# Kernel optimization log

Measured on AMD Instinct MI355X. Metric: run time of the kernel, lower is better.

The kernel has to match this reference:

```python
import jax, jax.numpy as jnp
import numpy as np

B, N = 8, 50000
DIM, C_DIM, TASK_DIM, H, NB, OUT = 3, 64, 512, 64, 5, 12


def setup_inputs() -> dict:
    key = jax.random.key(0)
    ks = jax.random.split(key, 16)
    s = lambda fan_in: 1.0 / np.sqrt(fan_in)
    inp = {
        "p": jax.random.normal(ks[0], (B, N, DIM), dtype=jnp.float32),
        "c": jax.random.normal(ks[1], (B, N, C_DIM), dtype=jnp.float32),
        "task_feature": jax.random.normal(ks[2], (B, TASK_DIM), dtype=jnp.float32),
        # params (stored as [in, out] so y = x @ W + b)
        "fc_p_W": jax.random.uniform(ks[3], (DIM, H), jnp.float32, -s(DIM), s(DIM)),
        "fc_p_b": jax.random.uniform(ks[4], (H,), jnp.float32, -s(DIM), s(DIM)),
        "fc_c_W": jax.random.uniform(ks[5], (NB, C_DIM + TASK_DIM, H), jnp.float32, -s(C_DIM + TASK_DIM), s(C_DIM + TASK_DIM)),
        "fc_c_b": jax.random.uniform(ks[6], (NB, H), jnp.float32, -s(C_DIM + TASK_DIM), s(C_DIM + TASK_DIM)),
        "blk0_W": jax.random.uniform(ks[7], (NB, H, H), jnp.float32, -s(H), s(H)),
        "blk0_b": jax.random.uniform(ks[8], (NB, H), jnp.float32, -s(H), s(H)),
        "blk1_W": jax.random.uniform(ks[9], (NB, H, H), jnp.float32, -s(H), s(H)) * 0.1,
        "blk1_b": jax.random.uniform(ks[10], (NB, H), jnp.float32, -s(H), s(H)),
        "fc_out_W": jax.random.uniform(ks[11], (H, OUT), jnp.float32, -s(H), s(H)),
        "fc_out_b": jax.random.uniform(ks[12], (OUT,), jnp.float32, -s(H), s(H)),
    }
    return inp


def reference(p, c, task_feature, fc_p_W, fc_p_b, fc_c_W, fc_c_b,
              blk0_W, blk0_b, blk1_W, blk1_b, fc_out_W, fc_out_b):
    b, n = p.shape[0], p.shape[1]
    # expand task feature to every point and concat with point-wise code c
    tf = jnp.broadcast_to(task_feature[:, None, :], (b, n, task_feature.shape[-1]))
    cc = jnp.concatenate([c, tf], axis=-1)              # [B, N, 576]
    net = p @ fc_p_W + fc_p_b                           # [B, N, H]
    for i in range(fc_c_W.shape[0]):
        net = net + cc @ fc_c_W[i] + fc_c_b[i]          # conditioning
        # ResnetBlockFC: dx = fc_1(relu(fc_0(relu(x)))); out = x + dx
        h = jax.nn.relu(net) @ blk0_W[i] + blk0_b[i]
        dx = jax.nn.relu(h) @ blk1_W[i] + blk1_b[i]
        net = net + dx
    out = jax.nn.relu(net) @ fc_out_W + fc_out_b        # [B, N, 12]
    return out
```

## Files before the change

kernel.cpp:

```cpp
#include <hip/hip_runtime.h>

#define B_    8
#define N_    50000
#define NB_   5
#define OUT_  12
#define THREADS 256
#define TILES_ 4
#define PTS_PER_BLOCK (TILES_ * 16 * 4)
#define BLOCKS_PER_BATCH ((N_ + PTS_PER_BLOCK - 1) / PTS_PER_BLOCK)

typedef _Float16 half8 __attribute__((ext_vector_type(8)));
typedef float   floatx4 __attribute__((ext_vector_type(4)));

__device__ __forceinline__ half8 ldg8(const _Float16* p) {
    union { uint4 u; half8 h; } x;
    x.u = *(const uint4*)p;
    return x.h;
}

__device__ __forceinline__ half8 packB(floatx4 a, floatx4 b) {
    half8 r;
    r[0] = (_Float16)fmaxf(a[0], 0.f); r[1] = (_Float16)fmaxf(a[1], 0.f);
    r[2] = (_Float16)fmaxf(a[2], 0.f); r[3] = (_Float16)fmaxf(a[3], 0.f);
    r[4] = (_Float16)fmaxf(b[0], 0.f); r[5] = (_Float16)fmaxf(b[1], 0.f);
    r[6] = (_Float16)fmaxf(b[2], 0.f); r[7] = (_Float16)fmaxf(b[3], 0.f);
    return r;
}

__global__ void task_proj_kernel(const float* __restrict__ tf,
                                 const float* __restrict__ fc_c_W,
                                 const float* __restrict__ fc_c_b,
                                 const float* __restrict__ fc_p_b,
                                 float* __restrict__ tp_out) {
    __shared__ float partial[4][64];
    int bi = blockIdx.x;
    int b = bi / NB_, i = bi % NB_;
    int j = threadIdx.x & 63;
    int g = threadIdx.x >> 6;
    const float* W  = fc_c_W + ((size_t)i * 576 + 64) * 64;
    const float* tb = tf + b * 512;
    float acc = 0.f;
    int t0 = g * 128;
    #pragma unroll 8
    for (int t = 0; t < 128; ++t)
        acc += tb[t0 + t] * W[(size_t)(t0 + t) * 64 + j];
    partial[g][j] = acc;
    __syncthreads();
    if (g == 0) {
        float s = partial[0][j] + partial[1][j] + partial[2][j] + partial[3][j]
                + fc_c_b[i * 64 + j];
        if (i == 0) s += fc_p_b[j];
        tp_out[(b * NB_ + i) * 64 + j] = s;
    }
}

__global__ void prep_weights(const float* __restrict__ fc_c_W,
                             const float* __restrict__ blk0_W,
                             const float* __restrict__ blk1_W,
                             const float* __restrict__ fc_out_W,
                             _Float16* __restrict__ ws_w,
                             _Float16* __restrict__ ws_fco) {
    int u = blockIdx.x * THREADS + threadIdx.x;
    if (u < 7680) {
        int m15 = u & 15, q = (u >> 4) & 3, h = (u >> 6) & 1, T = (u >> 7) & 3;
        int mi = u >> 9;
        int mat = mi / 5, i = mi % 5;
        int n = T * 16 + m15;
        _Float16 out[8];
        #pragma unroll
        for (int j = 0; j < 8; ++j) {
            float v;
            if (mat == 0) {
                int k = 32 * h + 8 * q + j;
                v = fc_c_W[((size_t)i * 576 + k) * 64 + n];
            } else {
                int f = 32 * h + 16 * (j >> 2) + 4 * q + (j & 3);
                const float* W = (mat == 1) ? blk0_W : blk1_W;
                v = W[((size_t)i * 64 + f) * 64 + n];
            }
            out[j] = (_Float16)v;
        }
        *(uint4*)(ws_w + (size_t)u * 8) = *(uint4*)out;
    } else if (u < 7808) {
        int e = u - 7680;
        int m15 = e & 15, q = (e >> 4) & 3, h = (e >> 6) & 1;
        _Float16 out[8];
        #pragma unroll
        for (int j = 0; j < 8; ++j) {
            int f = 32 * h + 16 * (j >> 2) + 4 * q + (j & 3);
            out[j] = (m15 < OUT_) ? (_Float16)fc_out_W[f * OUT_ + m15] : (_Float16)0.f;
        }
        *(uint4*)(ws_fco + (size_t)e * 8) = *(uint4*)out;
    }
}

__global__ __launch_bounds__(THREADS, 2) void decoder_kernel(
    const float* __restrict__ p_g, const float* __restrict__ c_g,
    const float* __restrict__ blk0_b, const float* __restrict__ blk1_b,
    const float* __restrict__ fc_p_W, const float* __restrict__ fc_out_b,
    const _Float16* __restrict__ ws_w, const _Float16* __restrict__ ws_fco,
    const float* __restrict__ ws_tp, float* __restrict__ out_g)
{
    __shared__ float fpw_l[192];
    __shared__ float b0_l[NB_ * 64];
    __shared__ float b1_l[NB_ * 64];
    __shared__ float tp_l[NB_ * 64];
    __shared__ float fob_l[16];

    const int tid   = threadIdx.x;
    const int batch = blockIdx.x / BLOCKS_PER_BATCH;
    const int blk   = blockIdx.x % BLOCKS_PER_BATCH;
    const int base  = blk * PTS_PER_BLOCK;
    const int npts  = min(PTS_PER_BLOCK, N_ - base);
    const int ntiles = npts >> 4;
    const long gbase = (long)batch * N_ + base;

    if (tid < 192) fpw_l[tid] = fc_p_W[tid];
    for (int u = tid; u < NB_ * 64; u += THREADS) {
        b0_l[u] = blk0_b[u];
        b1_l[u] = blk1_b[u];
        tp_l[u] = ws_tp[batch * (NB_ * 64) + u];
    }
    if (tid < 16) fob_l[tid] = (tid < OUT_) ? fc_out_b[tid] : 0.f;
    __syncthreads();

    const int lane = tid & 63;
    const int wv   = tid >> 6;
    const int q    = lane >> 4;
    const int m15  = lane & 15;

    int tileid[TILES_];
    bool act[TILES_];
    #pragma unroll
    for (int t = 0; t < TILES_; ++t) {
        tileid[t] = wv + 4 * t;
        act[t] = (tileid[t] < ntiles);
    }

    half8 cB[TILES_][2];
    #pragma unroll
    for (int t = 0; t < TILES_; ++t) {
        if (!act[t]) continue;
        const float* cr = c_g + (size_t)(gbase + tileid[t] * 16 + m15) * 64;
        #pragma unroll
        for (int h = 0; h < 2; ++h) {
            float4 v0 = *(const float4*)(cr + 32 * h + 8 * q);
            float4 v1 = *(const float4*)(cr + 32 * h + 8 * q + 4);
            half8 r;
            r[0] = (_Float16)v0.x; r[1] = (_Float16)v0.y;
            r[2] = (_Float16)v0.z; r[3] = (_Float16)v0.w;
            r[4] = (_Float16)v1.x; r[5] = (_Float16)v1.y;
            r[6] = (_Float16)v1.z; r[7] = (_Float16)v1.w;
            cB[t][h] = r;
        }
    }

    floatx4 net4[TILES_][4];
    #pragma unroll
    for (int t = 0; t < TILES_; ++t) {
        if (!act[t]) continue;
        long g = gbase + tileid[t] * 16 + m15;
        float pp0 = p_g[g * 3 + 0], pp1 = p_g[g * 3 + 1], pp2 = p_g[g * 3 + 2];
        #pragma unroll
        for (int T = 0; T < 4; ++T) {
            #pragma unroll
            for (int r = 0; r < 4; ++r) {
                int f = (T << 4) + (q << 2) + r;
                net4[t][T][r] = pp0 * fpw_l[f] + pp1 * fpw_l[64 + f] + pp2 * fpw_l[128 + f];
            }
        }
    }

    #pragma unroll 1
    for (int i = 0; i < NB_; ++i) {
        floatx4 tpv[4], bb0[4], bb1[4];
        #pragma unroll
        for (int T = 0; T < 4; ++T) {
            int off = i * 64 + (T << 4) + (q << 2);
            tpv[T] = *(const floatx4*)(tp_l + off);
            bb0[T] = *(const floatx4*)(b0_l + off);
            bb1[T] = *(const floatx4*)(b1_l + off);
        }
        {
            const _Float16* wbase = ws_w + ((size_t)(0 * 5 + i) * 512) * 8;
            half8 A[4][2];
            #pragma unroll
            for (int T = 0; T < 4; ++T)
                #pragma unroll
                for (int h = 0; h < 2; ++h)
                    A[T][h] = ldg8(wbase + ((T * 128 + h * 64 + q * 16 + m15) * 8));
            #pragma unroll
            for (int t = 0; t < TILES_; ++t) {
                if (!act[t]) continue;
                #pragma unroll
                for (int T = 0; T < 4; ++T) {
                    floatx4 a = net4[t][T];
                    a = __builtin_amdgcn_mfma_f32_16x16x32_f16(A[T][0], cB[t][0], a, 0, 0, 0);
                    a = __builtin_amdgcn_mfma_f32_16x16x32_f16(A[T][1], cB[t][1], a, 0, 0, 0);
                    net4[t][T] = a + tpv[T];
                }
            }
        }
        {
            const _Float16* w0 = ws_w + ((size_t)(1 * 5 + i) * 512) * 8;
            const _Float16* w1 = ws_w + ((size_t)(2 * 5 + i) * 512) * 8;
            half8 A0[4][2], A1[4][2];
            #pragma unroll
            for (int T = 0; T < 4; ++T)
                #pragma unroll
                for (int h = 0; h < 2; ++h) {
                    int off = (T * 128 + h * 64 + q * 16 + m15) * 8;
                    A0[T][h] = ldg8(w0 + off);
                    A1[T][h] = ldg8(w1 + off);
                }
            #pragma unroll
            for (int t = 0; t < TILES_; ++t) {
                if (!act[t]) continue;
                half8 Bn0 = packB(net4[t][0], net4[t][1]);
                half8 Bn1 = packB(net4[t][2], net4[t][3]);
                floatx4 hh[4];
                #pragma unroll
                for (int T = 0; T < 4; ++T) {
                    floatx4 a = bb0[T];
                    a = __builtin_amdgcn_mfma_f32_16x16x32_f16(A0[T][0], Bn0, a, 0, 0, 0);
                    a = __builtin_amdgcn_mfma_f32_16x16x32_f16(A0[T][1], Bn1, a, 0, 0, 0);
                    hh[T] = a;
                }
                half8 Bh0 = packB(hh[0], hh[1]);
                half8 Bh1 = packB(hh[2], hh[3]);
                #pragma unroll
                for (int T = 0; T < 4; ++T) {
                    floatx4 a = bb1[T];
                    a = __builtin_amdgcn_mfma_f32_16x16x32_f16(A1[T][0], Bh0, a, 0, 0, 0);
                    a = __builtin_amdgcn_mfma_f32_16x16x32_f16(A1[T][1], Bh1, a, 0, 0, 0);
                    net4[t][T] += a;
                }
            }
        }
    }

    half8 Ao0 = ldg8(ws_fco + (0 * 64 + q * 16 + m15) * 8);
    half8 Ao1 = ldg8(ws_fco + (1 * 64 + q * 16 + m15) * 8);
    floatx4 ob;
    #pragma unroll
    for (int r = 0; r < 4; ++r) ob[r] = fob_l[(q << 2) + r];
    #pragma unroll
    for (int t = 0; t < TILES_; ++t) {
        if (!act[t]) continue;
        half8 Bn0 = packB(net4[t][0], net4[t][1]);
        half8 Bn1 = packB(net4[t][2], net4[t][3]);
        floatx4 a = ob;
        a = __builtin_amdgcn_mfma_f32_16x16x32_f16(Ao0, Bn0, a, 0, 0, 0);
        a = __builtin_amdgcn_mfma_f32_16x16x32_f16(Ao1, Bn1, a, 0, 0, 0);
        if (q < 3) {
            long g = gbase + tileid[t] * 16 + m15;
            *(float4*)(out_g + g * OUT_ + (q << 2)) = make_float4(a[0], a[1], a[2], a[3]);
        }
    }
}

extern "C" void kernel_launch(void* const* d_in, const int* in_sizes, int n_in,
                              void* d_out, int out_size, void* d_ws, size_t ws_size,
                              hipStream_t stream) {
    const float* p        = (const float*)d_in[0];
    const float* c        = (const float*)d_in[1];
    const float* tf       = (const float*)d_in[2];
    const float* fc_p_W   = (const float*)d_in[3];
    const float* fc_p_b   = (const float*)d_in[4];
    const float* fc_c_W   = (const float*)d_in[5];
    const float* fc_c_b   = (const float*)d_in[6];
    const float* blk0_W   = (const float*)d_in[7];
    const float* blk0_b   = (const float*)d_in[8];
    const float* blk1_W   = (const float*)d_in[9];
    const float* blk1_b   = (const float*)d_in[10];
    const float* fc_out_W = (const float*)d_in[11];
    const float* fc_out_b = (const float*)d_in[12];
    float* out = (float*)d_out;

    _Float16* ws_w   = (_Float16*)d_ws;
    _Float16* ws_fco = ws_w + 7680 * 8;
    float*    ws_tp  = (float*)(ws_fco + 128 * 8);

    prep_weights<<<31, THREADS, 0, stream>>>(fc_c_W, blk0_W, blk1_W, fc_out_W, ws_w, ws_fco);
    task_proj_kernel<<<B_ * NB_, THREADS, 0, stream>>>(tf, fc_c_W, fc_c_b, fc_p_b, ws_tp);
    decoder_kernel<<<B_ * BLOCKS_PER_BATCH, THREADS, 0, stream>>>(
        p, c, blk0_b, blk1_b, fc_p_W, fc_out_b, ws_w, ws_fco, ws_tp, out);
}
```

Measured before the change: 247.7 us.

## Restructure decoder into single-wave blocks with double-buffered weight registers and replicated weights

The decoder now runs one 64-thread wave per block with four tiles each. Weight fragments are double-buffered in registers (X/Y) so the next matrix's loads are issued while the current MFMAs run. Biases and task projections are read straight from global memory instead of staged through LDS, which removes the barrier. The fp16 weight buffer is replicated up to 8 times across workspace to spread cache traffic. The task projection is split into more blocks plus a finalize kernel merged with weight prep. This raises register pressure and adds a launch and extra workspace writes.

Result: faster. 237.3 us (-4.2%).

```diff
diff --git a/kernel.cpp b/kernel.cpp
--- a/kernel.cpp
+++ b/kernel.cpp
@@ -4,10 +4,9 @@
 #define N_    50000
 #define NB_   5
 #define OUT_  12
-#define THREADS 256
 #define TILES_ 4
-#define PTS_PER_BLOCK (TILES_ * 16 * 4)
-#define BLOCKS_PER_BATCH ((N_ + PTS_PER_BLOCK - 1) / PTS_PER_BLOCK)
+#define TILES_PER_BATCH 3125
+#define BLOCKS_PER_BATCH 782
 
 typedef _Float16 half8 __attribute__((ext_vector_type(8)));
 typedef float   floatx4 __attribute__((ext_vector_type(4)));
@@ -27,121 +26,176 @@
     return r;
 }
 
-__global__ void task_proj_kernel(const float* __restrict__ tf,
-                                 const float* __restrict__ fc_c_W,
-                                 const float* __restrict__ fc_c_b,
-                                 const float* __restrict__ fc_p_b,
-                                 float* __restrict__ tp_out) {
-    __shared__ float partial[4][64];
-    int bi = blockIdx.x;
-    int b = bi / NB_, i = bi % NB_;
-    int j = threadIdx.x & 63;
-    int g = threadIdx.x >> 6;
-    const float* W  = fc_c_W + ((size_t)i * 576 + 64) * 64;
-    const float* tb = tf + b * 512;
-    float acc = 0.f;
-    int t0 = g * 128;
-    #pragma unroll 8
-    for (int t = 0; t < 128; ++t)
-        acc += tb[t0 + t] * W[(size_t)(t0 + t) * 64 + j];
-    partial[g][j] = acc;
-    __syncthreads();
-    if (g == 0) {
-        float s = partial[0][j] + partial[1][j] + partial[2][j] + partial[3][j]
-                + fc_c_b[i * 64 + j];
-        if (i == 0) s += fc_p_b[j];
-        tp_out[(b * NB_ + i) * 64 + j] = s;
-    }
-}
-
-__global__ void prep_weights(const float* __restrict__ fc_c_W,
-                             const float* __restrict__ blk0_W,
-                             const float* __restrict__ blk1_W,
-                             const float* __restrict__ fc_out_W,
-                             _Float16* __restrict__ ws_w,
-                             _Float16* __restrict__ ws_fco) {
-    int u = blockIdx.x * THREADS + threadIdx.x;
-    if (u < 7680) {
-        int m15 = u & 15, q = (u >> 4) & 3, h = (u >> 6) & 1, T = (u >> 7) & 3;
-        int mi = u >> 9;
-        int mat = mi / 5, i = mi % 5;
-        int n = T * 16 + m15;
-        _Float16 out[8];
-        #pragma unroll
-        for (int j = 0; j < 8; ++j) {
-            float v;
-            if (mat == 0) {
-                int k = 32 * h + 8 * q + j;
-                v = fc_c_W[((size_t)i * 576 + k) * 64 + n];
-            } else {
-                int f = 32 * h + 16 * (j >> 2) + 4 * q + (j & 3);
-                const float* W = (mat == 1) ? blk0_W : blk1_W;
-                v = W[((size_t)i * 64 + f) * 64 + n];
+__device__ __forceinline__ void load8(half8 (&A)[8], const _Float16* base, int q16m) {
+    #pragma unroll
+    for (int T = 0; T < 4; ++T)
+        #pragma unroll
+        for (int h = 0; h < 2; ++h)
+            A[T * 2 + h] = ldg8(base + (size_t)(T * 128 + h * 64 + q16m) * 8);
+}
+
+__global__ void prep_kernel(const float* __restrict__ fc_c_W,
+                            const float* __restrict__ blk0_W,
+                            const float* __restrict__ blk1_W,
+                            const float* __restrict__ fc_out_W,
+                            const float* __restrict__ tf,
+                            _Float16* __restrict__ ws_w,
+                            _Float16* __restrict__ ws_fco,
+                            float* __restrict__ partials, int R) {
+    int bid = blockIdx.x, tid = threadIdx.x;
+    if (bid < 32) {
+        int u = bid * 256 + tid;
+        if (u < 7680) {
+            int m15 = u & 15, q = (u >> 4) & 3, h = (u >> 6) & 1, T = (u >> 7) & 3;
+            int mi = u >> 9;
+            int mat = mi / 5, i = mi % 5;
+            int n = T * 16 + m15;
+            _Float16 out[8];
+            #pragma unroll
+            for (int j = 0; j < 8; ++j) {
+                float v;
+                if (mat == 0) {
+                    int k = 32 * h + 8 * q + j;
+                    v = fc_c_W[((size_t)i * 576 + k) * 64 + n];
+                } else {
+                    int f = 32 * h + 16 * (j >> 2) + 4 * q + (j & 3);
+                    const float* W = (mat == 1) ? blk0_W : blk1_W;
+                    v = W[((size_t)i * 64 + f) * 64 + n];
+                }
+                out[j] = (_Float16)v;
             }
-            out[j] = (_Float16)v;
-        }
-        *(uint4*)(ws_w + (size_t)u * 8) = *(uint4*)out;
-    } else if (u < 7808) {
-        int e = u - 7680;
-        int m15 = e & 15, q = (e >> 4) & 3, h = (e >> 6) & 1;
-        _Float16 out[8];
-        #pragma unroll
-        for (int j = 0; j < 8; ++j) {
-            int f = 32 * h + 16 * (j >> 2) + 4 * q + (j & 3);
-            out[j] = (m15 < OUT_) ? (_Float16)fc_out_W[f * OUT_ + m15] : (_Float16)0.f;
-        }
-        *(uint4*)(ws_fco + (size_t)e * 8) = *(uint4*)out;
-    }
-}
-
-__global__ __launch_bounds__(THREADS, 2) void decoder_kernel(
+            uint4 val = *(uint4*)out;
+            for (int r = 0; r < R; ++r)
+                *(uint4*)(ws_w + (size_t)r * 61440 + (size_t)u * 8) = val;
+        } else {
+            int e = u - 7680;
+            _Float16 out[8] = {};
+            if (e < 128) {
+                int m15 = e & 15, q = (e >> 4) & 3, h = (e >> 6) & 1;
+                #pragma unroll
+                for (int j = 0; j < 8; ++j) {
+                    int f = 32 * h + 16 * (j >> 2) + 4 * q + (j & 3);
+                    out[j] = (m15 < OUT_) ? (_Float16)fc_out_W[f * OUT_ + m15] : (_Float16)0.f;
+                }
+            }
+            uint4 val = *(uint4*)out;
+            for (int r = 0; r < R; ++r)
+                *(uint4*)(ws_fco + (size_t)r * 4096 + (size_t)e * 8) = val;
+        }
+    } else {
+        int idx2 = bid - 32;
+        int b = idx2 / 10, rem = idx2 % 10, i = rem >> 1, hf = rem & 1;
+        int g = tid >> 6, j = tid & 63;
+        const float* W  = fc_c_W + ((size_t)i * 576 + 64) * 64;
+        const float* tb = tf + b * 512;
+        int t0 = hf * 256 + g * 64;
+        float acc = 0.f;
+        #pragma unroll 8
+        for (int t = 0; t < 64; ++t)
+            acc += tb[t0 + t] * W[(size_t)(t0 + t) * 64 + j];
+        partials[(((b * 5 + i) << 3) + (hf * 4 + g)) * 64 + j] = acc;
+    }
+}
+
+__global__ void finalize_tp(const float* __restrict__ partials,
+                            const float* __restrict__ fc_c_b,
+                            const float* __restrict__ fc_p_b,
+                            float* __restrict__ tp) {
+    int u = blockIdx.x * 256 + threadIdx.x;
+    if (u >= 2560) return;
+    int b = u / 320, rem = u % 320, i = rem >> 6, j = rem & 63;
+    float s = fc_c_b[i * 64 + j] + ((i == 0) ? fc_p_b[j] : 0.f);
+    #pragma unroll
+    for (int k = 0; k < 8; ++k)
+        s += partials[(((b * 5 + i) << 3) + k) * 64 + j];
+    tp[u] = s;
+}
+
+__device__ __forceinline__ void resblock(
+    half8 (&Ac)[8], half8 (&Ab)[8],
+    floatx4 (&net4)[TILES_][4], const half8 (&cB)[TILES_][2],
+    int tc, int i, int q, int q16m,
+    const float* __restrict__ tp_b, const float* __restrict__ b0g,
+    const float* __restrict__ b1g, const _Float16* __restrict__ wsr,
+    const _Float16* __restrict__ next_cond_base, bool last)
+{
+    floatx4 tpv[4], bb0[4], bb1[4];
+    #pragma unroll
+    for (int T = 0; T < 4; ++T) {
+        int off = i * 64 + 16 * T + 4 * q;
+        tpv[T] = *(const floatx4*)(tp_b + off);
+        bb0[T] = *(const floatx4*)(b0g + off);
+        bb1[T] = *(const floatx4*)(b1g + off);
+    }
+    #pragma unroll
+    for (int t = 0; t < TILES_; ++t) {
+        if (t >= tc) break;
+        #pragma unroll
+        for (int T = 0; T < 4; ++T) {
+            floatx4 a = net4[t][T];
+            a = __builtin_amdgcn_mfma_f32_16x16x32_f16(Ac[2 * T], cB[t][0], a, 0, 0, 0);
+            a = __builtin_amdgcn_mfma_f32_16x16x32_f16(Ac[2 * T + 1], cB[t][1], a, 0, 0, 0);
+            net4[t][T] = a + tpv[T];
+        }
+    }
+    load8(Ac, wsr + (size_t)(10 + i) * 4096, q16m);
+    #pragma unroll
+    for (int t = 0; t < TILES_; ++t) {
+        if (t >= tc) break;
+        half8 Bn0 = packB(net4[t][0], net4[t][1]);
+        half8 Bn1 = packB(net4[t][2], net4[t][3]);
+        floatx4 hh[4];
+        #pragma unroll
+        for (int T = 0; T < 4; ++T) {
+            floatx4 a = bb0[T];
+            a = __builtin_amdgcn_mfma_f32_16x16x32_f16(Ab[2 * T], Bn0, a, 0, 0, 0);
+            a = __builtin_amdgcn_mfma_f32_16x16x32_f16(Ab[2 * T + 1], Bn1, a, 0, 0, 0);
+            hh[T] = a;
+        }
+        half8 Bh0 = packB(hh[0], hh[1]);
+        half8 Bh1 = packB(hh[2], hh[3]);
+        #pragma unroll
+        for (int T = 0; T < 4; ++T) {
+            floatx4 a = bb1[T];
+            a = __builtin_amdgcn_mfma_f32_16x16x32_f16(Ac[2 * T], Bh0, a, 0, 0, 0);
+            a = __builtin_amdgcn_mfma_f32_16x16x32_f16(Ac[2 * T + 1], Bh1, a, 0, 0, 0);
+            net4[t][T] += a;
+        }
+    }
+    load8(Ab, next_cond_base, q16m);
+    if (!last)
+        load8(Ac, wsr + (size_t)(5 + i + 1) * 4096, q16m);
+}
+
+__global__ __launch_bounds__(64, 2) void decoder_kernel(
     const float* __restrict__ p_g, const float* __restrict__ c_g,
     const float* __restrict__ blk0_b, const float* __restrict__ blk1_b,
     const float* __restrict__ fc_p_W, const float* __restrict__ fc_out_b,
     const _Float16* __restrict__ ws_w, const _Float16* __restrict__ ws_fco,
-    const float* __restrict__ ws_tp, float* __restrict__ out_g)
+    const float* __restrict__ tp_g, float* __restrict__ out_g, int rmask)
 {
-    __shared__ float fpw_l[192];
-    __shared__ float b0_l[NB_ * 64];
-    __shared__ float b1_l[NB_ * 64];
-    __shared__ float tp_l[NB_ * 64];
-    __shared__ float fob_l[16];
-
-    const int tid   = threadIdx.x;
-    const int batch = blockIdx.x / BLOCKS_PER_BATCH;
-    const int blk   = blockIdx.x % BLOCKS_PER_BATCH;
-    const int base  = blk * PTS_PER_BLOCK;
-    const int npts  = min(PTS_PER_BLOCK, N_ - base);
-    const int ntiles = npts >> 4;
-    const long gbase = (long)batch * N_ + base;
-
-    if (tid < 192) fpw_l[tid] = fc_p_W[tid];
-    for (int u = tid; u < NB_ * 64; u += THREADS) {
-        b0_l[u] = blk0_b[u];
-        b1_l[u] = blk1_b[u];
-        tp_l[u] = ws_tp[batch * (NB_ * 64) + u];
-    }
-    if (tid < 16) fob_l[tid] = (tid < OUT_) ? fc_out_b[tid] : 0.f;
-    __syncthreads();
-
-    const int lane = tid & 63;
-    const int wv   = tid >> 6;
-    const int q    = lane >> 4;
-    const int m15  = lane & 15;
-
-    int tileid[TILES_];
-    bool act[TILES_];
-    #pragma unroll
-    for (int t = 0; t < TILES_; ++t) {
-        tileid[t] = wv + 4 * t;
-        act[t] = (tileid[t] < ntiles);
-    }
+    const int bid   = blockIdx.x;
+    const int batch = bid / BLOCKS_PER_BATCH;
+    const int blk   = bid % BLOCKS_PER_BATCH;
+    const int tile0 = blk * TILES_;
+    const int tc    = min(TILES_, TILES_PER_BATCH - tile0);
+    const long gbase = (long)batch * N_ + (long)tile0 * 16;
+    const int lane = threadIdx.x;
+    const int q = lane >> 4, m15 = lane & 15;
+    const int q16m = q * 16 + m15;
+    const _Float16* wsr  = ws_w  + (size_t)(bid & rmask) * 61440;
+    const _Float16* fcor = ws_fco + (size_t)(bid & rmask) * 4096;
+    const float* tp_b = tp_g + batch * (NB_ * 64);
+
+    half8 X[8], Y[8];
+    load8(X, wsr, q16m);
+    load8(Y, wsr + (size_t)5 * 4096, q16m);
 
     half8 cB[TILES_][2];
     #pragma unroll
     for (int t = 0; t < TILES_; ++t) {
-        if (!act[t]) continue;
-        const float* cr = c_g + (size_t)(gbase + tileid[t] * 16 + m15) * 64;
+        if (t >= tc) break;
+        const float* cr = c_g + (size_t)(gbase + t * 16 + m15) * 64;
         #pragma unroll
         for (int h = 0; h < 2; ++h) {
             float4 v0 = *(const float4*)(cr + 32 * h + 8 * q);
@@ -155,106 +209,42 @@
         }
     }
 
+    floatx4 fw[3][4];
+    #pragma unroll
+    for (int d = 0; d < 3; ++d)
+        #pragma unroll
+        for (int T = 0; T < 4; ++T)
+            fw[d][T] = *(const floatx4*)(fc_p_W + d * 64 + 16 * T + 4 * q);
     floatx4 net4[TILES_][4];
     #pragma unroll
     for (int t = 0; t < TILES_; ++t) {
-        if (!act[t]) continue;
-        long g = gbase + tileid[t] * 16 + m15;
+        if (t >= tc) break;
+        long g = gbase + t * 16 + m15;
         float pp0 = p_g[g * 3 + 0], pp1 = p_g[g * 3 + 1], pp2 = p_g[g * 3 + 2];
         #pragma unroll
-        for (int T = 0; T < 4; ++T) {
-            #pragma unroll
-            for (int r = 0; r < 4; ++r) {
-                int f = (T << 4) + (q << 2) + r;
-                net4[t][T][r] = pp0 * fpw_l[f] + pp1 * fpw_l[64 + f] + pp2 * fpw_l[128 + f];
-            }
-        }
-    }
-
-    #pragma unroll 1
-    for (int i = 0; i < NB_; ++i) {
-        floatx4 tpv[4], bb0[4], bb1[4];
-        #pragma unroll
-        for (int T = 0; T < 4; ++T) {
-            int off = i * 64 + (T << 4) + (q << 2);
-            tpv[T] = *(const floatx4*)(tp_l + off);
-            bb0[T] = *(const floatx4*)(b0_l + off);
-            bb1[T] = *(const floatx4*)(b1_l + off);
-        }
-        {
-            const _Float16* wbase = ws_w + ((size_t)(0 * 5 + i) * 512) * 8;
-            half8 A[4][2];
-            #pragma unroll
-            for (int T = 0; T < 4; ++T)
-                #pragma unroll
-                for (int h = 0; h < 2; ++h)
-                    A[T][h] = ldg8(wbase + ((T * 128 + h * 64 + q * 16 + m15) * 8));
-            #pragma unroll
-            for (int t = 0; t < TILES_; ++t) {
-                if (!act[t]) continue;
-                #pragma unroll
-                for (int T = 0; T < 4; ++T) {
-                    floatx4 a = net4[t][T];
-                    a = __builtin_amdgcn_mfma_f32_16x16x32_f16(A[T][0], cB[t][0], a, 0, 0, 0);
-                    a = __builtin_amdgcn_mfma_f32_16x16x32_f16(A[T][1], cB[t][1], a, 0, 0, 0);
-                    net4[t][T] = a + tpv[T];
-                }
-            }
-        }
-        {
-            const _Float16* w0 = ws_w + ((size_t)(1 * 5 + i) * 512) * 8;
-            const _Float16* w1 = ws_w + ((size_t)(2 * 5 + i) * 512) * 8;
-            half8 A0[4][2], A1[4][2];
-            #pragma unroll
-            for (int T = 0; T < 4; ++T)
-                #pragma unroll
-                for (int h = 0; h < 2; ++h) {
-                    int off = (T * 128 + h * 64 + q * 16 + m15) * 8;
-                    A0[T][h] = ldg8(w0 + off);
-                    A1[T][h] = ldg8(w1 + off);
-                }
-            #pragma unroll
-            for (int t = 0; t < TILES_; ++t) {
-                if (!act[t]) continue;
-                half8 Bn0 = packB(net4[t][0], net4[t][1]);
-                half8 Bn1 = packB(net4[t][2], net4[t][3]);
-                floatx4 hh[4];
-                #pragma unroll
-                for (int T = 0; T < 4; ++T) {
-                    floatx4 a = bb0[T];
-                    a = __builtin_amdgcn_mfma_f32_16x16x32_f16(A0[T][0], Bn0, a, 0, 0, 0);
-                    a = __builtin_amdgcn_mfma_f32_16x16x32_f16(A0[T][1], Bn1, a, 0, 0, 0);
-                    hh[T] = a;
-                }
-                half8 Bh0 = packB(hh[0], hh[1]);
-                half8 Bh1 = packB(hh[2], hh[3]);
-                #pragma unroll
-                for (int T = 0; T < 4; ++T) {
-                    floatx4 a = bb1[T];
-                    a = __builtin_amdgcn_mfma_f32_16x16x32_f16(A1[T][0], Bh0, a, 0, 0, 0);
-                    a = __builtin_amdgcn_mfma_f32_16x16x32_f16(A1[T][1], Bh1, a, 0, 0, 0);
-                    net4[t][T] += a;
-                }
-            }
-        }
-    }
-
-    half8 Ao0 = ldg8(ws_fco + (0 * 64 + q * 16 + m15) * 8);
-    half8 Ao1 = ldg8(ws_fco + (1 * 64 + q * 16 + m15) * 8);
-    floatx4 ob;
-    #pragma unroll
-    for (int r = 0; r < 4; ++r) ob[r] = fob_l[(q << 2) + r];
-    #pragma unroll
-    for (int t = 0; t < TILES_; ++t) {
-        if (!act[t]) continue;
+        for (int T = 0; T < 4; ++T)
+            net4[t][T] = fw[0][T] * pp0 + fw[1][T] * pp1 + fw[2][T] * pp2;
+    }
+
+    resblock(X, Y, net4, cB, tc, 0, q, q16m, tp_b, blk0_b, blk1_b, wsr, wsr + (size_t)1 * 4096, false);
+    resblock(Y, X, net4, cB, tc, 1, q, q16m, tp_b, blk0_b, blk1_b, wsr, wsr + (size_t)2 * 4096, false);
+    resblock(X, Y, net4, cB, tc, 2, q, q16m, tp_b, blk0_b, blk1_b, wsr, wsr + (size_t)3 * 4096, false);
+    resblock(Y, X, net4, cB, tc, 3, q, q16m, tp_b, blk0_b, blk1_b, wsr, wsr + (size_t)4 * 4096, false);
+    resblock(X, Y, net4, cB, tc, 4, q, q16m, tp_b, blk0_b, blk1_b, wsr, fcor, true);
+
+    floatx4 ob = {0.f, 0.f, 0.f, 0.f};
+    if (q < 3) ob = *(const floatx4*)(fc_out_b + 4 * q);
+    #pragma unroll
+    for (int t = 0; t < TILES_; ++t) {
+        if (t >= tc) break;
         half8 Bn0 = packB(net4[t][0], net4[t][1]);
         half8 Bn1 = packB(net4[t][2], net4[t][3]);
         floatx4 a = ob;
-        a = __builtin_amdgcn_mfma_f32_16x16x32_f16(Ao0, Bn0, a, 0, 0, 0);
-        a = __builtin_amdgcn_mfma_f32_16x16x32_f16(Ao1, Bn1, a, 0, 0, 0);
+        a = __builtin_amdgcn_mfma_f32_16x16x32_f16(Y[0], Bn0, a, 0, 0, 0);
+        a = __builtin_amdgcn_mfma_f32_16x16x32_f16(Y[1], Bn1, a, 0, 0, 0);
         if (q < 3) {
-            long g = gbase + tileid[t] * 16 + m15;
-            *(float4*)(out_g + g * OUT_ + (q << 2)) = make_float4(a[0], a[1], a[2], a[3]);
+            long g = gbase + t * 16 + m15;
+            *(float4*)(out_g + g * OUT_ + 4 * q) = make_float4(a[0], a[1], a[2], a[3]);
         }
     }
 }
@@ -277,12 +267,17 @@
     const float* fc_out_b = (const float*)d_in[12];
     float* out = (float*)d_out;
 
+    int R = 8;
+    while (R > 1 && ((size_t)R * (61440 + 4096) * 2 + 81920 + 10240) > ws_size) R >>= 1;
+
     _Float16* ws_w   = (_Float16*)d_ws;
-    _Float16* ws_fco = ws_w + 7680 * 8;
-    float*    ws_tp  = (float*)(ws_fco + 128 * 8);
-
-    prep_weights<<<31, THREADS, 0, stream>>>(fc_c_W, blk0_W, blk1_W, fc_out_W, ws_w, ws_fco);
-    task_proj_kernel<<<B_ * NB_, THREADS, 0, stream>>>(tf, fc_c_W, fc_c_b, fc_p_b, ws_tp);
-    decoder_kernel<<<B_ * BLOCKS_PER_BATCH, THREADS, 0, stream>>>(
-        p, c, blk0_b, blk1_b, fc_p_W, fc_out_b, ws_w, ws_fco, ws_tp, out);
-}
+    _Float16* ws_fco = ws_w + (size_t)R * 61440;
+    float* partials  = (float*)(ws_fco + (size_t)R * 4096);
+    float* tp        = partials + 20480;
+
+    prep_kernel<<<112, 256, 0, stream>>>(fc_c_W, blk0_W, blk1_W, fc_out_W, tf,
+                                         ws_w, ws_fco, partials, R);
+    finalize_tp<<<10, 256, 0, stream>>>(partials, fc_c_b, fc_p_b, tp);
+    decoder_kernel<<<B_ * BLOCKS_PER_BATCH, 64, 0, stream>>>(
+        p, c, blk0_b, blk1_b, fc_p_W, fc_out_b, ws_w, ws_fco, tp, out, R - 1);
+}
```
